# Kernel tuning notes

Measured on AMD Instinct MI355X. Metric: run time of the kernel, lower is better.

Reference implementation:

```python
import jax, jax.numpy as jnp
import numpy as np

N = 524288
IN_C = 128
OUT_C = 128
NUM_GRAPHS = 64
NUM_STROKES = 8192
EPS = 1e-5


def setup_inputs() -> dict:
    key = jax.random.key(0)
    ks = jax.random.split(key, 8)
    x = jax.random.normal(ks[0], (N, IN_C), dtype=jnp.float32)
    batch = jnp.sort(jax.random.randint(ks[1], (N,), 0, NUM_GRAPHS))
    stroke_idx = jnp.sort(jax.random.randint(ks[2], (N,), 0, NUM_STROKES))
    s = 1.0 / np.sqrt(IN_C)
    W_max = jax.random.uniform(ks[3], (IN_C, OUT_C), jnp.float32, -s, s)
    b_max = jax.random.uniform(ks[4], (OUT_C,), jnp.float32, -s, s)
    g_max = jnp.ones((OUT_C,), jnp.float32)
    be_max = jnp.zeros((OUT_C,), jnp.float32)
    W_sk = jax.random.uniform(ks[5], (IN_C, OUT_C), jnp.float32, -s, s)
    b_sk = jax.random.uniform(ks[6], (OUT_C,), jnp.float32, -s, s)
    g_sk = jnp.ones((OUT_C,), jnp.float32)
    be_sk = jnp.zeros((OUT_C,), jnp.float32)
    return {"x": x, "batch": batch, "stroke_idx": stroke_idx,
            "W_max": W_max, "b_max": b_max, "g_max": g_max, "be_max": be_max,
            "W_sk": W_sk, "b_sk": b_sk, "g_sk": g_sk, "be_sk": be_sk}


def _mlp(x, W, b, gamma, beta):
    # Linear -> BatchNorm1d (training-mode batch stats, biased var) -> ReLU
    h = x @ W + b
    mu = jnp.mean(h, axis=0)
    var = jnp.mean((h - mu) ** 2, axis=0)
    h = (h - mu) * jax.lax.rsqrt(var + EPS) * gamma + beta
    return jax.nn.relu(h)


def reference(x, batch, stroke_idx, W_max, b_max, g_max, be_max, W_sk, b_sk, g_sk, be_sk):
    pool_max = _mlp(x, W_max, b_max, g_max, be_max)      # (N, F)
    pool_sketch = _mlp(x, W_sk, b_sk, g_sk, be_sk)       # (N, F)
    # segment max-pool per graph / per stroke, then broadcast back to nodes
    gmax = jax.ops.segment_max(pool_max, batch, num_segments=NUM_GRAPHS)       # (G, F)
    smax = jax.ops.segment_max(pool_sketch, stroke_idx, num_segments=NUM_STROKES)  # (S, F)
    pool_max = gmax[batch]          # (N, F)
    pool_sketch = smax[stroke_idx]  # (N, F)
    return jnp.concatenate([pool_sketch, pool_max], axis=1)  # (N, 2F)
```

## Files before the change

kernel.cpp:

```cpp
#include <hip/hip_runtime.h>
#include <hip/hip_bf16.h>
#include <climits>
#include <cstdint>
#include <cfloat>

#define NROWS   524288
#define KDIM    128
#define NGRAPH  64
#define NSTROKE 8192
#define EPSF    1e-5f

typedef __bf16 bf16x8 __attribute__((ext_vector_type(8)));
typedef float  f32x4  __attribute__((ext_vector_type(4)));
typedef unsigned short u16x4 __attribute__((ext_vector_type(4)));

#define WT_OFF    0
#define CSUM_OFF  65536
#define CSQ_OFF   66560
#define ST_OFF    67584
#define GT_OFF    (ST_OFF + NSTROKE*KDIM*4)

__device__ __forceinline__ unsigned short f2bf(float f) {
  unsigned int u = __float_as_uint(f);
  u += 0x7fffu + ((u >> 16) & 1u);
  return (unsigned short)(u >> 16);
}
__device__ __forceinline__ float bf2f(unsigned short u) {
  return __uint_as_float(((unsigned int)u) << 16);
}
__device__ __forceinline__ int fkey(float f) {
  int b = __float_as_int(f);
  return b >= 0 ? b : (b ^ 0x7fffffff);
}
__device__ __forceinline__ float fdec(int k) {
  int b = k >= 0 ? k : (k ^ 0x7fffffff);
  return __int_as_float(b);
}

__global__ void k_init(const float* __restrict__ Wmax, const float* __restrict__ Wsk,
                       unsigned char* __restrict__ ws) {
  unsigned short* wt = (unsigned short*)(ws + WT_OFF);
  float* csum = (float*)(ws + CSUM_OFF);
  float* csq  = (float*)(ws + CSQ_OFF);
  int* st = (int*)(ws + ST_OFF);
  int* gt = (int*)(ws + GT_OFF);
  int i = blockIdx.x * blockDim.x + threadIdx.x;
  const int total = NSTROKE * KDIM;
  for (; i < total; i += gridDim.x * blockDim.x) {
    st[i] = INT_MIN;
    if (i < NGRAPH * KDIM) gt[i] = INT_MIN;
    if (i < 256) { csum[i] = 0.f; csq[i] = 0.f; }
    if (i < 256 * KDIM) {
      int c = i / KDIM, k = i % KDIM;
      float w = (c < 128) ? Wsk[k * 128 + c] : Wmax[k * 128 + (c - 128)];
      wt[i] = f2bf(w);
    }
  }
}

__global__ __launch_bounds__(256) void k_pass1(const float* __restrict__ x,
                                               const int* __restrict__ batch,
                                               const int* __restrict__ stroke,
                                               unsigned char* __restrict__ ws) {
  __shared__ __align__(16) unsigned short xs[64 * 128];
  __shared__ __align__(16) unsigned short hs[256 * 64];
  __shared__ int ss[64];
  __shared__ int gg[64];
  const unsigned short* wt = (const unsigned short*)(ws + WT_OFF);
  float* csum = (float*)(ws + CSUM_OFF);
  float* csq  = (float*)(ws + CSQ_OFF);
  int* st = (int*)(ws + ST_OFF);
  int* gt = (int*)(ws + GT_OFF);

  const int tid  = threadIdx.x;
  const int lane = tid & 63;
  const int wv   = tid >> 6;
  const int lr   = lane & 15;
  const int lg   = lane >> 4;

  bf16x8 bfrag[4][4];
#pragma unroll
  for (int ks = 0; ks < 4; ++ks)
#pragma unroll
    for (int n = 0; n < 4; ++n) {
      int c = wv * 64 + n * 16 + lr;
      int k = ks * 32 + lg * 8;
      bfrag[ks][n] = *(const bf16x8*)(wt + c * KDIM + k);
    }

  float sumn[4] = {0.f, 0.f, 0.f, 0.f};
  float sqn[4]  = {0.f, 0.f, 0.f, 0.f};
  int* mp = (tid < 128) ? (st + tid) : (gt + (tid - 128));

  for (int ti = 0; ti < 8; ++ti) {
    const int row0 = (blockIdx.x * 8 + ti) * 64;

#pragma unroll
    for (int it = 0; it < 4; ++it) {
      int e  = it * 2048 + tid * 8;
      int r  = e >> 7;
      int kg = (e & 127) >> 3;
      const float* src = x + (size_t)(row0 + r) * KDIM + kg * 8;
      f32x4 v0 = *(const f32x4*)src;
      f32x4 v1 = *(const f32x4*)(src + 4);
      union { bf16x8 v; unsigned short u[8]; } pk;
      pk.u[0] = f2bf(v0[0]); pk.u[1] = f2bf(v0[1]); pk.u[2] = f2bf(v0[2]); pk.u[3] = f2bf(v0[3]);
      pk.u[4] = f2bf(v1[0]); pk.u[5] = f2bf(v1[1]); pk.u[6] = f2bf(v1[2]); pk.u[7] = f2bf(v1[3]);
      *(bf16x8*)(xs + r * KDIM + ((kg ^ (r & 7)) << 3)) = pk.v;
    }
    if (tid < 64)       ss[tid]      = stroke[row0 + tid];
    else if (tid < 128) gg[tid - 64] = batch[row0 + tid - 64];
    __syncthreads();

    f32x4 acc[4][4];
#pragma unroll
    for (int m = 0; m < 4; ++m)
#pragma unroll
      for (int n = 0; n < 4; ++n) { f32x4 z = {0.f, 0.f, 0.f, 0.f}; acc[m][n] = z; }

#pragma unroll
    for (int ks = 0; ks < 4; ++ks) {
      bf16x8 af[4];
#pragma unroll
      for (int m = 0; m < 4; ++m) {
        int r  = m * 16 + lr;
        int kg = ks * 4 + lg;
        af[m] = *(const bf16x8*)(xs + r * KDIM + ((kg ^ (r & 7)) << 3));
      }
#pragma unroll
      for (int m = 0; m < 4; ++m)
#pragma unroll
        for (int n = 0; n < 4; ++n)
          acc[m][n] = __builtin_amdgcn_mfma_f32_16x16x32_bf16(af[m], bfrag[ks][n], acc[m][n], 0, 0, 0);
    }

#pragma unroll
    for (int n = 0; n < 4; ++n) {
      float s = 0.f, q = 0.f;
#pragma unroll
      for (int m = 0; m < 4; ++m)
#pragma unroll
        for (int rg = 0; rg < 4; ++rg) { float v = acc[m][n][rg]; s += v; q = fmaf(v, v, q); }
      sumn[n] += s; sqn[n] += q;
    }

#pragma unroll
    for (int m = 0; m < 4; ++m)
#pragma unroll
      for (int n = 0; n < 4; ++n) {
        u16x4 p;
#pragma unroll
        for (int rg = 0; rg < 4; ++rg) p[rg] = f2bf(acc[m][n][rg]);
        int c    = wv * 64 + n * 16 + lr;
        int rowb = m * 16 + lg * 4;
        int byte = (c << 7) + (((rowb >> 3) ^ (c & 7)) << 4) + ((rowb & 7) << 1);
        *(u16x4*)((char*)hs + byte) = p;
      }
    __syncthreads();

    const int* segl = (tid < 128) ? ss : gg;
    int curseg = segl[0]; float runmax = -FLT_MAX;
#pragma unroll
    for (int J = 0; J < 8; ++J) {
      int byte = (tid << 7) + ((J ^ (tid & 7)) << 4);
      union { bf16x8 v; unsigned short u[8]; } hv;
      hv.v = *(const bf16x8*)((const char*)hs + byte);
#pragma unroll
      for (int rr = 0; rr < 8; ++rr) {
        float v = bf2f(hv.u[rr]);
        int seg = segl[J * 8 + rr];
        if (seg != curseg) {
          atomicMax(&mp[curseg * KDIM], fkey(runmax));
          curseg = seg; runmax = v;
        } else {
          runmax = fmaxf(runmax, v);
        }
      }
    }
    atomicMax(&mp[curseg * KDIM], fkey(runmax));
    __syncthreads();
  }

#pragma unroll
  for (int n = 0; n < 4; ++n) {
    sumn[n] += __shfl_xor(sumn[n], 16);
    sumn[n] += __shfl_xor(sumn[n], 32);
    sqn[n]  += __shfl_xor(sqn[n], 16);
    sqn[n]  += __shfl_xor(sqn[n], 32);
  }
  float s = 0.f, q = 0.f;
#pragma unroll
  for (int n = 0; n < 4; ++n) if (n == lg) { s = sumn[n]; q = sqn[n]; }
  atomicAdd(&csum[tid], s);
  atomicAdd(&csq[tid], q);
}

__global__ __launch_bounds__(256) void k_out(const int* __restrict__ batch,
                                             const int* __restrict__ stroke,
                                             const float* __restrict__ g_max,
                                             const float* __restrict__ be_max,
                                             const float* __restrict__ g_sk,
                                             const float* __restrict__ be_sk,
                                             const unsigned char* __restrict__ ws,
                                             float* __restrict__ out) {
  const float* csum = (const float*)(ws + CSUM_OFF);
  const float* csq  = (const float*)(ws + CSQ_OFF);
  const int* st = (const int*)(ws + ST_OFF);
  const int* gt = (const int*)(ws + GT_OFF);

  const int lane = threadIdx.x & 63;
  const int wvid = blockIdx.x * 4 + (threadIdx.x >> 6);
  const int row0 = wvid * 64;
  const bool isS = lane < 32;
  const int  cg  = (isS ? lane : lane - 32) * 4;
  const int* tab  = isS ? st : gt;
  const int* idxp = isS ? stroke : batch;
  const float* gv = isS ? g_sk : g_max;
  const float* bv = isS ? be_sk : be_max;

  const float invN = 1.0f / (float)NROWS;
  f32x4 mu, sc, bb;
#pragma unroll
  for (int j = 0; j < 4; ++j) {
    int cc = (isS ? 0 : 128) + cg + j;
    float m  = csum[cc] * invN;
    float vr = csq[cc] * invN - m * m;
    mu[j] = m;
    sc[j] = gv[cg + j] * rsqrtf(vr + EPSF);
    bb[j] = bv[cg + j];
  }

  f32x4* out4 = (f32x4*)out;
#pragma unroll 4
  for (int r = 0; r < 64; ++r) {
    int row = row0 + r;
    int seg = idxp[row];
    const int4 k4 = *(const int4*)(tab + (size_t)seg * KDIM + cg);
    f32x4 v;
    v[0] = fdec(k4.x); v[1] = fdec(k4.y); v[2] = fdec(k4.z); v[3] = fdec(k4.w);
#pragma unroll
    for (int j = 0; j < 4; ++j) v[j] = fmaxf(0.f, (v[j] - mu[j]) * sc[j] + bb[j]);
    __builtin_nontemporal_store(v, &out4[(size_t)row * 64 + lane]);
  }
}

extern "C" void kernel_launch(void* const* d_in, const int* in_sizes, int n_in,
                              void* d_out, int out_size, void* d_ws, size_t ws_size,
                              hipStream_t stream) {
  const float* x      = (const float*)d_in[0];
  const int*   batch  = (const int*)d_in[1];
  const int*   stroke = (const int*)d_in[2];
  const float* Wmax   = (const float*)d_in[3];
  const float* g_max  = (const float*)d_in[5];
  const float* be_max = (const float*)d_in[6];
  const float* Wsk    = (const float*)d_in[7];
  const float* g_sk   = (const float*)d_in[9];
  const float* be_sk  = (const float*)d_in[10];
  unsigned char* ws = (unsigned char*)d_ws;
  float* out = (float*)d_out;

  k_init <<<2048, 512, 0, stream>>>(Wmax, Wsk, ws);
  k_pass1<<<1024, 256, 0, stream>>>(x, batch, stroke, ws);
  k_out  <<<2048, 256, 0, stream>>>(batch, stroke, g_max, be_max, g_sk, be_sk, ws, out);
}
```

Baseline: 250.1 us.

## Software-pipeline x tile loads in pass1 with register double buffering

Restructures the pass1 loop so the next 64-row tile of x is loaded into registers (with nontemporal loads) while the current tile is computed with MFMA and reduced. Each block now handles 16 tiles instead of 8, with half as many blocks launched, and launch bounds request 2 blocks per CU. This targets global-load latency exposed between tiles. The extra prefetch registers raise register pressure, and the smaller grid may lower occupancy or cause load imbalance.

```diff
diff --git a/kernel.cpp b/kernel.cpp
--- a/kernel.cpp
+++ b/kernel.cpp
@@ -58,10 +58,114 @@
   }
 }
 
-__global__ __launch_bounds__(256) void k_pass1(const float* __restrict__ x,
-                                               const int* __restrict__ batch,
-                                               const int* __restrict__ stroke,
-                                               unsigned char* __restrict__ ws) {
+#define TILES1 16
+
+#define LOADT(PF, ROW0)                                                  \
+  {                                                                      \
+    const float* srcb = x + (size_t)(ROW0) * KDIM;                       \
+    _Pragma("unroll")                                                    \
+    for (int it = 0; it < 4; ++it) {                                     \
+      int r  = it * 16 + (tid >> 4);                                     \
+      int kg = tid & 15;                                                 \
+      const f32x4* src = (const f32x4*)(srcb + r * KDIM + kg * 8);       \
+      PF##_0[it] = __builtin_nontemporal_load(src);                      \
+      PF##_1[it] = __builtin_nontemporal_load(src + 1);                  \
+    }                                                                    \
+  }
+
+#define SEGLD(SR, ROW0)                                                  \
+  if (tid < 128) SR = ((tid < 64) ? stroke : batch)[(ROW0) + (tid & 63)];
+
+#define STORET(PF, SR)                                                   \
+  {                                                                      \
+    _Pragma("unroll")                                                    \
+    for (int it = 0; it < 4; ++it) {                                     \
+      int r  = it * 16 + (tid >> 4);                                     \
+      int kg = tid & 15;                                                 \
+      union { bf16x8 v; unsigned short u[8]; } pk;                       \
+      f32x4 v0 = PF##_0[it], v1 = PF##_1[it];                            \
+      pk.u[0]=f2bf(v0[0]); pk.u[1]=f2bf(v0[1]);                          \
+      pk.u[2]=f2bf(v0[2]); pk.u[3]=f2bf(v0[3]);                          \
+      pk.u[4]=f2bf(v1[0]); pk.u[5]=f2bf(v1[1]);                          \
+      pk.u[6]=f2bf(v1[2]); pk.u[7]=f2bf(v1[3]);                          \
+      *(bf16x8*)(xs + r * KDIM + ((kg ^ (r & 7)) << 3)) = pk.v;          \
+    }                                                                    \
+    if (tid < 64) ss[tid] = SR; else if (tid < 128) gg[tid & 63] = SR;   \
+  }
+
+#define COMPUTE()                                                        \
+  {                                                                      \
+    f32x4 acc[4][4];                                                     \
+    _Pragma("unroll")                                                    \
+    for (int m = 0; m < 4; ++m)                                          \
+      _Pragma("unroll")                                                  \
+      for (int n = 0; n < 4; ++n) { f32x4 z = {0.f,0.f,0.f,0.f}; acc[m][n] = z; } \
+    _Pragma("unroll")                                                    \
+    for (int ks = 0; ks < 4; ++ks) {                                     \
+      bf16x8 af[4];                                                      \
+      _Pragma("unroll")                                                  \
+      for (int m = 0; m < 4; ++m) {                                      \
+        int r  = m * 16 + lr;                                            \
+        int kg = ks * 4 + lg;                                            \
+        af[m] = *(const bf16x8*)(xs + r * KDIM + ((kg ^ (r & 7)) << 3)); \
+      }                                                                  \
+      _Pragma("unroll")                                                  \
+      for (int m = 0; m < 4; ++m)                                        \
+        _Pragma("unroll")                                                \
+        for (int n = 0; n < 4; ++n)                                      \
+          acc[m][n] = __builtin_amdgcn_mfma_f32_16x16x32_bf16(af[m], bfrag[ks][n], acc[m][n], 0, 0, 0); \
+    }                                                                    \
+    _Pragma("unroll")                                                    \
+    for (int n = 0; n < 4; ++n) {                                        \
+      float s = 0.f, q = 0.f;                                            \
+      _Pragma("unroll")                                                  \
+      for (int m = 0; m < 4; ++m)                                        \
+        _Pragma("unroll")                                                \
+        for (int rg = 0; rg < 4; ++rg) { float v = acc[m][n][rg]; s += v; q = fmaf(v, v, q); } \
+      sumn[n] += s; sqn[n] += q;                                         \
+    }                                                                    \
+    _Pragma("unroll")                                                    \
+    for (int m = 0; m < 4; ++m)                                          \
+      _Pragma("unroll")                                                  \
+      for (int n = 0; n < 4; ++n) {                                      \
+        u16x4 p;                                                         \
+        _Pragma("unroll")                                                \
+        for (int rg = 0; rg < 4; ++rg) p[rg] = f2bf(acc[m][n][rg]);      \
+        int c    = wv * 64 + n * 16 + lr;                                \
+        int rowb = m * 16 + lg * 4;                                      \
+        int byte = (c << 7) + (((rowb >> 3) ^ (c & 7)) << 4) + ((rowb & 7) << 1); \
+        *(u16x4*)((char*)hs + byte) = p;                                 \
+      }                                                                  \
+  }
+
+#define REDUCE()                                                         \
+  {                                                                      \
+    const int* segl = (tid < 128) ? ss : gg;                             \
+    int curseg = segl[0]; float runmax = -FLT_MAX;                       \
+    _Pragma("unroll")                                                    \
+    for (int J = 0; J < 8; ++J) {                                        \
+      int byte = (tid << 7) + ((J ^ (tid & 7)) << 4);                    \
+      union { bf16x8 v; unsigned short u[8]; } hv;                       \
+      hv.v = *(const bf16x8*)((const char*)hs + byte);                   \
+      _Pragma("unroll")                                                  \
+      for (int rr = 0; rr < 8; ++rr) {                                   \
+        float v = bf2f(hv.u[rr]);                                        \
+        int seg = segl[J * 8 + rr];                                      \
+        if (seg != curseg) {                                             \
+          atomicMax(&mp[curseg * KDIM], fkey(runmax));                   \
+          curseg = seg; runmax = v;                                      \
+        } else {                                                         \
+          runmax = fmaxf(runmax, v);                                     \
+        }                                                                \
+      }                                                                  \
+    }                                                                    \
+    atomicMax(&mp[curseg * KDIM], fkey(runmax));                         \
+  }
+
+__global__ __launch_bounds__(256, 2) void k_pass1(const float* __restrict__ x,
+                                                  const int* __restrict__ batch,
+                                                  const int* __restrict__ stroke,
+                                                  unsigned char* __restrict__ ws) {
   __shared__ __align__(16) unsigned short xs[64 * 128];
   __shared__ __align__(16) unsigned short hs[256 * 64];
   __shared__ int ss[64];
@@ -92,92 +196,28 @@
   float sqn[4]  = {0.f, 0.f, 0.f, 0.f};
   int* mp = (tid < 128) ? (st + tid) : (gt + (tid - 128));
 
-  for (int ti = 0; ti < 8; ++ti) {
-    const int row0 = (blockIdx.x * 8 + ti) * 64;
-
-#pragma unroll
-    for (int it = 0; it < 4; ++it) {
-      int e  = it * 2048 + tid * 8;
-      int r  = e >> 7;
-      int kg = (e & 127) >> 3;
-      const float* src = x + (size_t)(row0 + r) * KDIM + kg * 8;
-      f32x4 v0 = *(const f32x4*)src;
-      f32x4 v1 = *(const f32x4*)(src + 4);
-      union { bf16x8 v; unsigned short u[8]; } pk;
-      pk.u[0] = f2bf(v0[0]); pk.u[1] = f2bf(v0[1]); pk.u[2] = f2bf(v0[2]); pk.u[3] = f2bf(v0[3]);
-      pk.u[4] = f2bf(v1[0]); pk.u[5] = f2bf(v1[1]); pk.u[6] = f2bf(v1[2]); pk.u[7] = f2bf(v1[3]);
-      *(bf16x8*)(xs + r * KDIM + ((kg ^ (r & 7)) << 3)) = pk.v;
-    }
-    if (tid < 64)       ss[tid]      = stroke[row0 + tid];
-    else if (tid < 128) gg[tid - 64] = batch[row0 + tid - 64];
-    __syncthreads();
-
-    f32x4 acc[4][4];
-#pragma unroll
-    for (int m = 0; m < 4; ++m)
-#pragma unroll
-      for (int n = 0; n < 4; ++n) { f32x4 z = {0.f, 0.f, 0.f, 0.f}; acc[m][n] = z; }
-
-#pragma unroll
-    for (int ks = 0; ks < 4; ++ks) {
-      bf16x8 af[4];
-#pragma unroll
-      for (int m = 0; m < 4; ++m) {
-        int r  = m * 16 + lr;
-        int kg = ks * 4 + lg;
-        af[m] = *(const bf16x8*)(xs + r * KDIM + ((kg ^ (r & 7)) << 3));
-      }
-#pragma unroll
-      for (int m = 0; m < 4; ++m)
-#pragma unroll
-        for (int n = 0; n < 4; ++n)
-          acc[m][n] = __builtin_amdgcn_mfma_f32_16x16x32_bf16(af[m], bfrag[ks][n], acc[m][n], 0, 0, 0);
-    }
-
-#pragma unroll
-    for (int n = 0; n < 4; ++n) {
-      float s = 0.f, q = 0.f;
-#pragma unroll
-      for (int m = 0; m < 4; ++m)
-#pragma unroll
-        for (int rg = 0; rg < 4; ++rg) { float v = acc[m][n][rg]; s += v; q = fmaf(v, v, q); }
-      sumn[n] += s; sqn[n] += q;
-    }
-
-#pragma unroll
-    for (int m = 0; m < 4; ++m)
-#pragma unroll
-      for (int n = 0; n < 4; ++n) {
-        u16x4 p;
-#pragma unroll
-        for (int rg = 0; rg < 4; ++rg) p[rg] = f2bf(acc[m][n][rg]);
-        int c    = wv * 64 + n * 16 + lr;
-        int rowb = m * 16 + lg * 4;
-        int byte = (c << 7) + (((rowb >> 3) ^ (c & 7)) << 4) + ((rowb & 7) << 1);
-        *(u16x4*)((char*)hs + byte) = p;
-      }
-    __syncthreads();
-
-    const int* segl = (tid < 128) ? ss : gg;
-    int curseg = segl[0]; float runmax = -FLT_MAX;
-#pragma unroll
-    for (int J = 0; J < 8; ++J) {
-      int byte = (tid << 7) + ((J ^ (tid & 7)) << 4);
-      union { bf16x8 v; unsigned short u[8]; } hv;
-      hv.v = *(const bf16x8*)((const char*)hs + byte);
-#pragma unroll
-      for (int rr = 0; rr < 8; ++rr) {
-        float v = bf2f(hv.u[rr]);
-        int seg = segl[J * 8 + rr];
-        if (seg != curseg) {
-          atomicMax(&mp[curseg * KDIM], fkey(runmax));
-          curseg = seg; runmax = v;
-        } else {
-          runmax = fmaxf(runmax, v);
-        }
-      }
-    }
-    atomicMax(&mp[curseg * KDIM], fkey(runmax));
+  const int brow = blockIdx.x * (TILES1 * 64);
+
+  f32x4 pf0_0[4], pf0_1[4], pf1_0[4], pf1_1[4];
+  int seg0 = 0, seg1 = 0;
+  LOADT(pf0, brow);
+  SEGLD(seg0, brow);
+
+  for (int t4 = 0; t4 < TILES1 / 2; ++t4) {
+    const int tB = t4 * 2 + 1;
+    STORET(pf0, seg0);
+    __syncthreads();
+    { int rn = brow + tB * 64; LOADT(pf1, rn); SEGLD(seg1, rn); }
+    COMPUTE();
+    __syncthreads();
+    REDUCE();
+    __syncthreads();
+    STORET(pf1, seg1);
+    __syncthreads();
+    if (tB + 1 < TILES1) { int rn = brow + (tB + 1) * 64; LOADT(pf0, rn); SEGLD(seg0, rn); }
+    COMPUTE();
+    __syncthreads();
+    REDUCE();
     __syncthreads();
   }
 
@@ -260,6 +300,6 @@
   float* out = (float*)d_out;
 
   k_init <<<2048, 512, 0, stream>>>(Wmax, Wsk, ws);
-  k_pass1<<<1024, 256, 0, stream>>>(x, batch, stroke, ws);
+  k_pass1<<<512, 256, 0, stream>>>(x, batch, stroke, ws);
   k_out  <<<2048, 256, 0, stream>>>(batch, stroke, g_max, be_max, g_sk, be_sk, ws, out);
 }
```

Result: slower. 274.0 us (+9.5%).

## Restructure pass1: 8 waves, double-buffered x tiles, register-level segment max

Applied to the files above, without the earlier changes.

Grows pass1 blocks to 512 threads, with each wave owning 32 output columns. The x tile staging is double-buffered, so the global loads for the next tile overlap the MFMA work on the current one. The bf16 shared-memory round trip of h for the segment max is removed: per-column maxima are reduced in registers using ballot-detected segment boundaries and wave shuffles, then flushed with far fewer atomics. This cuts LDS traffic and a barrier per tile, at the cost of extra register pressure and a divergent path when a tile spans several segments.

```diff
diff --git a/kernel.cpp b/kernel.cpp
--- a/kernel.cpp
+++ b/kernel.cpp
@@ -12,7 +12,6 @@
 
 typedef __bf16 bf16x8 __attribute__((ext_vector_type(8)));
 typedef float  f32x4  __attribute__((ext_vector_type(4)));
-typedef unsigned short u16x4 __attribute__((ext_vector_type(4)));
 
 #define WT_OFF    0
 #define CSUM_OFF  65536
@@ -25,9 +24,6 @@
   u += 0x7fffu + ((u >> 16) & 1u);
   return (unsigned short)(u >> 16);
 }
-__device__ __forceinline__ float bf2f(unsigned short u) {
-  return __uint_as_float(((unsigned int)u) << 16);
-}
 __device__ __forceinline__ int fkey(float f) {
   int b = __float_as_int(f);
   return b >= 0 ? b : (b ^ 0x7fffffff);
@@ -35,6 +31,12 @@
 __device__ __forceinline__ float fdec(int k) {
   int b = k >= 0 ? k : (k ^ 0x7fffffff);
   return __int_as_float(b);
+}
+__device__ __forceinline__ bf16x8 cvt8(f32x4 a, f32x4 b) {
+  bf16x8 r;
+  r[0] = (__bf16)a[0]; r[1] = (__bf16)a[1]; r[2] = (__bf16)a[2]; r[3] = (__bf16)a[3];
+  r[4] = (__bf16)b[0]; r[5] = (__bf16)b[1]; r[6] = (__bf16)b[2]; r[7] = (__bf16)b[3];
+  return r;
 }
 
 __global__ void k_init(const float* __restrict__ Wmax, const float* __restrict__ Wsk,
@@ -58,14 +60,11 @@
   }
 }
 
-__global__ __launch_bounds__(256) void k_pass1(const float* __restrict__ x,
-                                               const int* __restrict__ batch,
-                                               const int* __restrict__ stroke,
-                                               unsigned char* __restrict__ ws) {
-  __shared__ __align__(16) unsigned short xs[64 * 128];
-  __shared__ __align__(16) unsigned short hs[256 * 64];
-  __shared__ int ss[64];
-  __shared__ int gg[64];
+__global__ __launch_bounds__(512, 4) void k_pass1(const float* __restrict__ x,
+                                                  const int* __restrict__ batch,
+                                                  const int* __restrict__ stroke,
+                                                  unsigned char* __restrict__ ws) {
+  __shared__ __align__(16) unsigned short xs[2][64 * 128];
   const unsigned short* wt = (const unsigned short*)(ws + WT_OFF);
   float* csum = (float*)(ws + CSUM_OFF);
   float* csq  = (float*)(ws + CSQ_OFF);
@@ -74,49 +73,78 @@
 
   const int tid  = threadIdx.x;
   const int lane = tid & 63;
-  const int wv   = tid >> 6;
+  const int w    = tid >> 6;
   const int lr   = lane & 15;
   const int lg   = lane >> 4;
-
-  bf16x8 bfrag[4][4];
+  const int colbase = w * 32;
+  const bool isS = (w < 4);
+  const int* __restrict__ segp = isS ? stroke : batch;
+  int* __restrict__ tab = isS ? st : gt;
+  const int tcol = colbase - (isS ? 0 : 128);
+
+  bf16x8 bfrag[4][2];
 #pragma unroll
   for (int ks = 0; ks < 4; ++ks)
 #pragma unroll
-    for (int n = 0; n < 4; ++n) {
-      int c = wv * 64 + n * 16 + lr;
-      int k = ks * 32 + lg * 8;
-      bfrag[ks][n] = *(const bf16x8*)(wt + c * KDIM + k);
-    }
-
-  float sumn[4] = {0.f, 0.f, 0.f, 0.f};
-  float sqn[4]  = {0.f, 0.f, 0.f, 0.f};
-  int* mp = (tid < 128) ? (st + tid) : (gt + (tid - 128));
-
-  for (int ti = 0; ti < 8; ++ti) {
-    const int row0 = (blockIdx.x * 8 + ti) * 64;
-
-#pragma unroll
-    for (int it = 0; it < 4; ++it) {
-      int e  = it * 2048 + tid * 8;
-      int r  = e >> 7;
-      int kg = (e & 127) >> 3;
-      const float* src = x + (size_t)(row0 + r) * KDIM + kg * 8;
-      f32x4 v0 = *(const f32x4*)src;
-      f32x4 v1 = *(const f32x4*)(src + 4);
-      union { bf16x8 v; unsigned short u[8]; } pk;
-      pk.u[0] = f2bf(v0[0]); pk.u[1] = f2bf(v0[1]); pk.u[2] = f2bf(v0[2]); pk.u[3] = f2bf(v0[3]);
-      pk.u[4] = f2bf(v1[0]); pk.u[5] = f2bf(v1[1]); pk.u[6] = f2bf(v1[2]); pk.u[7] = f2bf(v1[3]);
-      *(bf16x8*)(xs + r * KDIM + ((kg ^ (r & 7)) << 3)) = pk.v;
-    }
-    if (tid < 64)       ss[tid]      = stroke[row0 + tid];
-    else if (tid < 128) gg[tid - 64] = batch[row0 + tid - 64];
-    __syncthreads();
-
-    f32x4 acc[4][4];
+    for (int n = 0; n < 2; ++n)
+      bfrag[ks][n] = *(const bf16x8*)(wt + (colbase + n * 16 + lr) * KDIM + ks * 32 + lg * 8);
+
+  const int srow = tid >> 3;
+  const int su   = tid & 7;
+  const int brow = blockIdx.x * 512;
+
+  float sumn[2] = {0.f, 0.f};
+  float sqn[2]  = {0.f, 0.f};
+  float tmax0 = -FLT_MAX, tmax1 = -FLT_MAX;
+  int   curseg = -1;
+
+#define FLUSH()                                                               \
+  if (curseg >= 0) {                                                          \
+    float f0 = tmax0, f1 = tmax1;                                             \
+    f0 = fmaxf(f0, __shfl_xor(f0, 16)); f0 = fmaxf(f0, __shfl_xor(f0, 32));   \
+    f1 = fmaxf(f1, __shfl_xor(f1, 16)); f1 = fmaxf(f1, __shfl_xor(f1, 32));   \
+    if (lg == 0) {                                                            \
+      atomicMax(&tab[curseg * KDIM + tcol + lr],      fkey(f0));              \
+      atomicMax(&tab[curseg * KDIM + tcol + 16 + lr], fkey(f1));              \
+    }                                                                         \
+  }
+
+#define STAGE_LD(T)                                                           \
+  {                                                                           \
+    const float* src_ = x + (size_t)(brow + (T) * 64 + srow) * KDIM + su * 16;\
+    ld0 = *(const f32x4*)(src_);                                              \
+    ld1 = *(const f32x4*)(src_ + 4);                                          \
+    ld2 = *(const f32x4*)(src_ + 8);                                          \
+    ld3 = *(const f32x4*)(src_ + 12);                                         \
+  }
+#define STAGE_WR(P)                                                           \
+  {                                                                           \
+    unsigned short* xb_ = xs[P];                                              \
+    int kg0 = su * 2;                                                         \
+    *(bf16x8*)(xb_ + srow * KDIM + (((kg0    ) ^ (srow & 7)) << 3)) = cvt8(ld0, ld1); \
+    *(bf16x8*)(xb_ + srow * KDIM + (((kg0 + 1) ^ (srow & 7)) << 3)) = cvt8(ld2, ld3); \
+  }
+
+  f32x4 ld0, ld1, ld2, ld3;
+  STAGE_LD(0);
+  int segNext = segp[brow + lane];
+  STAGE_WR(0);
+  __syncthreads();
+
+  for (int t = 0; t < 8; ++t) {
+    const unsigned short* xb = xs[t & 1];
+    const int segLane = segNext;
+
+    if (t < 7) {
+      STAGE_LD(t + 1);
+      segNext = segp[brow + (t + 1) * 64 + lane];
+    }
+
+    f32x4 acc[4][2];
 #pragma unroll
     for (int m = 0; m < 4; ++m)
 #pragma unroll
-      for (int n = 0; n < 4; ++n) { f32x4 z = {0.f, 0.f, 0.f, 0.f}; acc[m][n] = z; }
+      for (int n = 0; n < 2; ++n) { f32x4 z = {0.f, 0.f, 0.f, 0.f}; acc[m][n] = z; }
 
 #pragma unroll
     for (int ks = 0; ks < 4; ++ks) {
@@ -125,74 +153,85 @@
       for (int m = 0; m < 4; ++m) {
         int r  = m * 16 + lr;
         int kg = ks * 4 + lg;
-        af[m] = *(const bf16x8*)(xs + r * KDIM + ((kg ^ (r & 7)) << 3));
+        af[m] = *(const bf16x8*)(xb + r * KDIM + ((kg ^ (r & 7)) << 3));
       }
 #pragma unroll
-      for (int m = 0; m < 4; ++m)
-#pragma unroll
-        for (int n = 0; n < 4; ++n)
-          acc[m][n] = __builtin_amdgcn_mfma_f32_16x16x32_bf16(af[m], bfrag[ks][n], acc[m][n], 0, 0, 0);
-    }
-
-#pragma unroll
-    for (int n = 0; n < 4; ++n) {
-      float s = 0.f, q = 0.f;
-#pragma unroll
-      for (int m = 0; m < 4; ++m)
-#pragma unroll
-        for (int rg = 0; rg < 4; ++rg) { float v = acc[m][n][rg]; s += v; q = fmaf(v, v, q); }
-      sumn[n] += s; sqn[n] += q;
-    }
-
+      for (int m = 0; m < 4; ++m) {
+        acc[m][0] = __builtin_amdgcn_mfma_f32_16x16x32_bf16(af[m], bfrag[ks][0], acc[m][0], 0, 0, 0);
+        acc[m][1] = __builtin_amdgcn_mfma_f32_16x16x32_bf16(af[m], bfrag[ks][1], acc[m][1], 0, 0, 0);
+      }
+    }
+
+    float s0 = 0.f, q0 = 0.f, s1 = 0.f, q1 = 0.f;
+    float t0 = -FLT_MAX, t1 = -FLT_MAX;
 #pragma unroll
     for (int m = 0; m < 4; ++m)
 #pragma unroll
-      for (int n = 0; n < 4; ++n) {
-        u16x4 p;
-#pragma unroll
-        for (int rg = 0; rg < 4; ++rg) p[rg] = f2bf(acc[m][n][rg]);
-        int c    = wv * 64 + n * 16 + lr;
-        int rowb = m * 16 + lg * 4;
-        int byte = (c << 7) + (((rowb >> 3) ^ (c & 7)) << 4) + ((rowb & 7) << 1);
-        *(u16x4*)((char*)hs + byte) = p;
+      for (int rg = 0; rg < 4; ++rg) {
+        float v0 = acc[m][0][rg], v1 = acc[m][1][rg];
+        s0 += v0; q0 = fmaf(v0, v0, q0); t0 = fmaxf(t0, v0);
+        s1 += v1; q1 = fmaf(v1, v1, q1); t1 = fmaxf(t1, v1);
       }
-    __syncthreads();
-
-    const int* segl = (tid < 128) ? ss : gg;
-    int curseg = segl[0]; float runmax = -FLT_MAX;
-#pragma unroll
-    for (int J = 0; J < 8; ++J) {
-      int byte = (tid << 7) + ((J ^ (tid & 7)) << 4);
-      union { bf16x8 v; unsigned short u[8]; } hv;
-      hv.v = *(const bf16x8*)((const char*)hs + byte);
-#pragma unroll
-      for (int rr = 0; rr < 8; ++rr) {
-        float v = bf2f(hv.u[rr]);
-        int seg = segl[J * 8 + rr];
-        if (seg != curseg) {
-          atomicMax(&mp[curseg * KDIM], fkey(runmax));
-          curseg = seg; runmax = v;
+    sumn[0] += s0; sqn[0] += q0; sumn[1] += s1; sqn[1] += q1;
+
+    {
+      int pv = __shfl_up(segLane, 1);
+      unsigned long long mask = __ballot(lane > 0 && pv != segLane);
+      if (mask == 0ull) {
+        int seg0 = __shfl(segLane, 0);
+        if (seg0 != curseg) {
+          FLUSH();
+          curseg = seg0; tmax0 = t0; tmax1 = t1;
         } else {
-          runmax = fmaxf(runmax, v);
+          tmax0 = fmaxf(tmax0, t0); tmax1 = fmaxf(tmax1, t1);
+        }
+      } else {
+        unsigned long long rem = mask;
+        int a = 0;
+        while (true) {
+          int b = rem ? (int)__builtin_ctzll(rem) : 64;
+          int segr = __shfl(segLane, a);
+          float r0 = -FLT_MAX, r1 = -FLT_MAX;
+#pragma unroll
+          for (int m = 0; m < 4; ++m)
+#pragma unroll
+            for (int rg = 0; rg < 4; ++rg) {
+              int row = m * 16 + lg * 4 + rg;
+              bool in = (row >= a) && (row < b);
+              r0 = in ? fmaxf(r0, acc[m][0][rg]) : r0;
+              r1 = in ? fmaxf(r1, acc[m][1][rg]) : r1;
+            }
+          if (a == 0 && segr == curseg) {
+            tmax0 = fmaxf(tmax0, r0); tmax1 = fmaxf(tmax1, r1);
+          } else {
+            FLUSH();
+            curseg = segr; tmax0 = r0; tmax1 = r1;
+          }
+          if (b >= 64) break;
+          rem &= rem - 1; a = b;
         }
       }
     }
-    atomicMax(&mp[curseg * KDIM], fkey(runmax));
+
+    if (t < 7) STAGE_WR((t + 1) & 1);
     __syncthreads();
   }
 
-#pragma unroll
-  for (int n = 0; n < 4; ++n) {
-    sumn[n] += __shfl_xor(sumn[n], 16);
-    sumn[n] += __shfl_xor(sumn[n], 32);
-    sqn[n]  += __shfl_xor(sqn[n], 16);
-    sqn[n]  += __shfl_xor(sqn[n], 32);
-  }
-  float s = 0.f, q = 0.f;
-#pragma unroll
-  for (int n = 0; n < 4; ++n) if (n == lg) { s = sumn[n]; q = sqn[n]; }
-  atomicAdd(&csum[tid], s);
-  atomicAdd(&csq[tid], q);
+  FLUSH();
+
+#pragma unroll
+  for (int n = 0; n < 2; ++n) {
+    float s = sumn[n], q = sqn[n];
+    s += __shfl_xor(s, 16); s += __shfl_xor(s, 32);
+    q += __shfl_xor(q, 16); q += __shfl_xor(q, 32);
+    if (lg == 0) {
+      atomicAdd(&csum[colbase + n * 16 + lr], s);
+      atomicAdd(&csq [colbase + n * 16 + lr], q);
+    }
+  }
+#undef FLUSH
+#undef STAGE_LD
+#undef STAGE_WR
 }
 
 __global__ __launch_bounds__(256) void k_out(const int* __restrict__ batch,
@@ -260,6 +299,6 @@
   float* out = (float*)d_out;
 
   k_init <<<2048, 512, 0, stream>>>(Wmax, Wsk, ws);
-  k_pass1<<<1024, 256, 0, stream>>>(x, batch, stroke, ws);
+  k_pass1<<<1024, 512, 0, stream>>>(x, batch, stroke, ws);
   k_out  <<<2048, 256, 0, stream>>>(batch, stroke, g_max, be_max, g_sk, be_sk, ws, out);
 }
```

New measurement: 294.2 us. 1.18x slower.

## Compute segment max directly from MFMA accumulators with wave ballot

Applied to the files above, without the earlier changes.

Replaces the LDS round-trip (bf16 store of the GEMM tile to shared memory, barrier, per-thread column scan) with an in-register segmented max. Each wave detects segment boundaries across its 64 rows via ballot, reduces over the accumulator fragments, and combines lanes with shuffles before issuing atomics. It keeps a running max across tiles, so atomics are issued only at segment changes. This removes a shared buffer, a barrier and bf16 rounding before the max, but adds a divergent boundary loop when a tile spans multiple strokes.

```diff
diff --git a/kernel.cpp b/kernel.cpp
--- a/kernel.cpp
+++ b/kernel.cpp
@@ -12,7 +12,6 @@
 
 typedef __bf16 bf16x8 __attribute__((ext_vector_type(8)));
 typedef float  f32x4  __attribute__((ext_vector_type(4)));
-typedef unsigned short u16x4 __attribute__((ext_vector_type(4)));
 
 #define WT_OFF    0
 #define CSUM_OFF  65536
@@ -24,9 +23,6 @@
   unsigned int u = __float_as_uint(f);
   u += 0x7fffu + ((u >> 16) & 1u);
   return (unsigned short)(u >> 16);
-}
-__device__ __forceinline__ float bf2f(unsigned short u) {
-  return __uint_as_float(((unsigned int)u) << 16);
 }
 __device__ __forceinline__ int fkey(float f) {
   int b = __float_as_int(f);
@@ -63,9 +59,6 @@
                                                const int* __restrict__ stroke,
                                                unsigned char* __restrict__ ws) {
   __shared__ __align__(16) unsigned short xs[64 * 128];
-  __shared__ __align__(16) unsigned short hs[256 * 64];
-  __shared__ int ss[64];
-  __shared__ int gg[64];
   const unsigned short* wt = (const unsigned short*)(ws + WT_OFF);
   float* csum = (float*)(ws + CSUM_OFF);
   float* csq  = (float*)(ws + CSQ_OFF);
@@ -90,7 +83,25 @@
 
   float sumn[4] = {0.f, 0.f, 0.f, 0.f};
   float sqn[4]  = {0.f, 0.f, 0.f, 0.f};
-  int* mp = (tid < 128) ? (st + tid) : (gt + (tid - 128));
+
+  const bool isS = (wv < 2);
+  const int* __restrict__ segp = isS ? stroke : batch;
+  int* __restrict__ tab = isS ? st : gt;
+  const int tcol = (isS ? wv : wv - 2) * 64;
+
+  int   curseg = -1;
+  float runmax[4] = {-FLT_MAX, -FLT_MAX, -FLT_MAX, -FLT_MAX};
+
+#define FLUSH()                                                               \
+  if (curseg >= 0) {                                                          \
+    _Pragma("unroll")                                                         \
+    for (int n = 0; n < 4; ++n) {                                             \
+      float f = runmax[n];                                                    \
+      f = fmaxf(f, __shfl_xor(f, 16));                                        \
+      f = fmaxf(f, __shfl_xor(f, 32));                                        \
+      if (lg == 0) atomicMax(&tab[curseg * KDIM + tcol + n * 16 + lr], fkey(f)); \
+    }                                                                         \
+  }
 
   for (int ti = 0; ti < 8; ++ti) {
     const int row0 = (blockIdx.x * 8 + ti) * 64;
@@ -108,8 +119,7 @@
       pk.u[4] = f2bf(v1[0]); pk.u[5] = f2bf(v1[1]); pk.u[6] = f2bf(v1[2]); pk.u[7] = f2bf(v1[3]);
       *(bf16x8*)(xs + r * KDIM + ((kg ^ (r & 7)) << 3)) = pk.v;
     }
-    if (tid < 64)       ss[tid]      = stroke[row0 + tid];
-    else if (tid < 128) gg[tid - 64] = batch[row0 + tid - 64];
+    int segv = segp[row0 + lane];
     __syncthreads();
 
     f32x4 acc[4][4];
@@ -134,52 +144,69 @@
           acc[m][n] = __builtin_amdgcn_mfma_f32_16x16x32_bf16(af[m], bfrag[ks][n], acc[m][n], 0, 0, 0);
     }
 
+    float tm[4];
 #pragma unroll
     for (int n = 0; n < 4; ++n) {
-      float s = 0.f, q = 0.f;
+      float s = 0.f, q = 0.f, t = -FLT_MAX;
 #pragma unroll
       for (int m = 0; m < 4; ++m)
 #pragma unroll
-        for (int rg = 0; rg < 4; ++rg) { float v = acc[m][n][rg]; s += v; q = fmaf(v, v, q); }
-      sumn[n] += s; sqn[n] += q;
-    }
-
-#pragma unroll
-    for (int m = 0; m < 4; ++m)
-#pragma unroll
-      for (int n = 0; n < 4; ++n) {
-        u16x4 p;
-#pragma unroll
-        for (int rg = 0; rg < 4; ++rg) p[rg] = f2bf(acc[m][n][rg]);
-        int c    = wv * 64 + n * 16 + lr;
-        int rowb = m * 16 + lg * 4;
-        int byte = (c << 7) + (((rowb >> 3) ^ (c & 7)) << 4) + ((rowb & 7) << 1);
-        *(u16x4*)((char*)hs + byte) = p;
-      }
-    __syncthreads();
-
-    const int* segl = (tid < 128) ? ss : gg;
-    int curseg = segl[0]; float runmax = -FLT_MAX;
-#pragma unroll
-    for (int J = 0; J < 8; ++J) {
-      int byte = (tid << 7) + ((J ^ (tid & 7)) << 4);
-      union { bf16x8 v; unsigned short u[8]; } hv;
-      hv.v = *(const bf16x8*)((const char*)hs + byte);
-#pragma unroll
-      for (int rr = 0; rr < 8; ++rr) {
-        float v = bf2f(hv.u[rr]);
-        int seg = segl[J * 8 + rr];
-        if (seg != curseg) {
-          atomicMax(&mp[curseg * KDIM], fkey(runmax));
-          curseg = seg; runmax = v;
+        for (int rg = 0; rg < 4; ++rg) {
+          float v = acc[m][n][rg];
+          s += v; q = fmaf(v, v, q); t = fmaxf(t, v);
+        }
+      sumn[n] += s; sqn[n] += q; tm[n] = t;
+    }
+
+    {
+      int pv = __shfl_up(segv, 1);
+      unsigned long long mask = __ballot(lane > 0 && pv != segv);
+      if (mask == 0ull) {
+        int seg0 = __shfl(segv, 0);
+        if (seg0 == curseg) {
+#pragma unroll
+          for (int n = 0; n < 4; ++n) runmax[n] = fmaxf(runmax[n], tm[n]);
         } else {
-          runmax = fmaxf(runmax, v);
+          FLUSH();
+          curseg = seg0;
+#pragma unroll
+          for (int n = 0; n < 4; ++n) runmax[n] = tm[n];
+        }
+      } else {
+        unsigned long long rem = mask;
+        int a = 0;
+        while (true) {
+          int b = rem ? (int)__builtin_ctzll(rem) : 64;
+          int segr = __shfl(segv, a);
+          float rm[4] = {-FLT_MAX, -FLT_MAX, -FLT_MAX, -FLT_MAX};
+#pragma unroll
+          for (int m = 0; m < 4; ++m)
+#pragma unroll
+            for (int rg = 0; rg < 4; ++rg) {
+              int pos = m * 16 + lg * 4 + rg;
+              bool in = (pos >= a) && (pos < b);
+#pragma unroll
+              for (int n = 0; n < 4; ++n)
+                rm[n] = in ? fmaxf(rm[n], acc[m][n][rg]) : rm[n];
+            }
+          if (a == 0 && segr == curseg) {
+#pragma unroll
+            for (int n = 0; n < 4; ++n) runmax[n] = fmaxf(runmax[n], rm[n]);
+          } else {
+            FLUSH();
+            curseg = segr;
+#pragma unroll
+            for (int n = 0; n < 4; ++n) runmax[n] = rm[n];
+          }
+          if (b >= 64) break;
+          rem &= rem - 1; a = b;
         }
       }
     }
-    atomicMax(&mp[curseg * KDIM], fkey(runmax));
     __syncthreads();
   }
+
+  FLUSH();
 
 #pragma unroll
   for (int n = 0; n < 4; ++n) {
@@ -193,6 +220,7 @@
   for (int n = 0; n < 4; ++n) if (n == lg) { s = sumn[n]; q = sqn[n]; }
   atomicAdd(&csum[tid], s);
   atomicAdd(&csq[tid], q);
+#undef FLUSH
 }
 
 __global__ __launch_bounds__(256) void k_out(const int* __restrict__ batch,
```

Result: no change. 248.4 us (-0.7%).
